# Optimization experiments

Hardware: AMD Instinct MI355X
Metric: run time of the kernel (lower is better)

Reference implementation:

```python
import jax, jax.numpy as jnp
import numpy as np

D, H, DH, W = 1280, 16, 80, 64  # d_model, heads, head_dim, window

def setup_inputs() -> dict:
    key = jax.random.key(0)
    ks = jax.random.split(key, 5)
    s, b = 4096, 8
    x = jax.random.normal(ks[0], (s, b, D), dtype=jnp.float32)
    cu_seqlens = jnp.arange(s // W + 1, dtype=jnp.int64) * W  # ignored by module
    qkv_w = jax.random.normal(ks[1], (3 * D, D), dtype=jnp.float32) * 0.02
    qkv_b = jnp.zeros((3 * D,), dtype=jnp.float32)
    proj_w = jax.random.normal(ks[2], (D, W * DH), dtype=jnp.float32) * 0.02
    proj_b = jnp.zeros((D,), dtype=jnp.float32)
    return {"x": x, "cu_seqlens": cu_seqlens, "qkv_w": qkv_w, "qkv_b": qkv_b,
            "proj_w": proj_w, "proj_b": proj_b}

def reference(x, cu_seqlens, qkv_w, qkv_b, proj_w, proj_b):
    s, b, _ = x.shape
    nw = s // W
    qkv = x @ qkv_w.T + qkv_b                       # (s, b, 3D)
    q, k, v = jnp.split(qkv, 3, axis=2)             # each (s, b, D)
    def prep(t):
        # (s,b,D) -> (b,s,H,DH) -> (b,nw,W,H,DH)
        return t.reshape(s, b, H, DH).transpose(1, 0, 2, 3).reshape(b, nw, W, H, DH)
    q, k, v = prep(q), prep(k), prep(v)
    scale = 1.0 / jnp.sqrt(jnp.array(DH, dtype=x.dtype))
    # Faithful to source: SDPA sees (b, heads=W, seq=H, dim=DH) per window,
    # i.e. attention over the 16-head axis with the 64 window positions as heads.
    scores = jnp.einsum('bnwhd,bnwgd->bnwhg', q, k) * scale   # (b,nw,W,H,H)
    attn = jax.nn.softmax(scores, axis=-1)
    out = jnp.einsum('bnwhg,bnwgd->bnwhd', attn, v)           # (b,nw,W,H,DH)
    # rearrange 'b h s d -> b s h d' per window, then concat over windows (dim=1)
    out = out.transpose(0, 1, 3, 2, 4).reshape(b, nw * H, W * DH)  # (b, nw*H, W*DH)
    out = out.transpose(1, 0, 2)                                    # (nw*H, b, 5120)
    return out @ proj_w.T + proj_b                                  # (nw*H, b, D)
```

## Files before the change

kernel.cpp:

```cpp
#include <hip/hip_runtime.h>
#include <hip/hip_bf16.h>
#include <stdint.h>

typedef __hip_bfloat16 bf16;
typedef __attribute__((ext_vector_type(8))) short short8;
typedef __attribute__((ext_vector_type(4))) float f32x4;

#define S_LEN   4096
#define BATCH   8
#define D_MODEL 1280
#define NHEADS  16
#define DHEAD   80
#define WIN     64
#define NWIN    (S_LEN / WIN)
#define QKV_N   (3 * D_MODEL)
#define ATT_K   (WIN * DHEAD)
#define M_QKV   (S_LEN * BATCH)
#define M_PROJ  (NWIN * NHEADS * BATCH)
#define OUT_ELEMS ((size_t)M_PROJ * D_MODEL)

#define NX4   (M_QKV * D_MODEL / 4)
#define NQW4  (QKV_N * D_MODEL / 4)
#define NPW4  (D_MODEL * ATT_K / 4)
#define NQB4  (QKV_N / 4)
#define NPB4  (D_MODEL / 4)
#define TOT4  (NX4 + NQW4 + NPW4 + NQB4 + NPB4)

__device__ __forceinline__ float bf2f(unsigned short b) {
    union { unsigned int i; float f; } v;
    v.i = ((unsigned int)b) << 16;
    return v.f;
}

__device__ __forceinline__ unsigned short f2bf(float f) {
    __hip_bfloat16 h = __float2bfloat16(f);
    return *reinterpret_cast<unsigned short*>(&h);
}

__global__ void detect_dtype(const unsigned short* __restrict__ x,
                             int* __restrict__ flag) {
    const int lane = threadIdx.x;
    int big = 0;
    for (int j = lane; j < 256; j += 64) {
        unsigned short u = x[2 * j];
        int e = (u >> 7) & 0xFF;
        big += (e >= 135) ? 1 : 0;
    }
#pragma unroll
    for (int m = 1; m < 64; m <<= 1) big += __shfl_xor(big, m, 64);
    if (lane == 0) *flag = (big >= 8) ? 1 : 0;
}

__global__ __launch_bounds__(256) void canon_all(
    const void* __restrict__ x,  const void* __restrict__ qw,
    const void* __restrict__ pw, const void* __restrict__ qb,
    const void* __restrict__ pb,
    bf16* __restrict__ xc, bf16* __restrict__ qwc, bf16* __restrict__ pwc,
    bf16* __restrict__ qbc, bf16* __restrict__ pbc,
    const int* __restrict__ flag) {
    const int f = *flag;
    const long i = (long)blockIdx.x * 256 + threadIdx.x;
    if (i >= TOT4) return;
    const void* src; bf16* dst; long j;
    if (i < NX4)                        { src = x;  dst = xc;  j = i; }
    else if (i < NX4 + NQW4)            { src = qw; dst = qwc; j = i - NX4; }
    else if (i < NX4 + NQW4 + NPW4)     { src = pw; dst = pwc; j = i - NX4 - NQW4; }
    else if (i < NX4 + NQW4 + NPW4 + NQB4) { src = qb; dst = qbc; j = i - NX4 - NQW4 - NPW4; }
    else                                { src = pb; dst = pbc; j = i - NX4 - NQW4 - NPW4 - NQB4; }
    if (f) {
        const float4 v = ((const float4*)src)[j];
        ushort4 o;
        o.x = f2bf(v.x); o.y = f2bf(v.y); o.z = f2bf(v.z); o.w = f2bf(v.w);
        ((ushort4*)dst)[j] = o;
    } else {
        ((ushort4*)dst)[j] = ((const ushort4*)src)[j];
    }
}

__device__ __forceinline__ void gload16(const bf16* g, bf16* l) {
    __builtin_amdgcn_global_load_lds(
        (const __attribute__((address_space(1))) void*)g,
        (__attribute__((address_space(3))) void*)l, 16, 0, 0);
}

__global__ __launch_bounds__(512) void gemm_bt_bias_256(
    const bf16* __restrict__ A, const bf16* __restrict__ B,
    const bf16* __restrict__ bias, void* __restrict__ Cout,
    int M, int N, int K, const int* __restrict__ out_f32)
{
    __shared__ bf16 sA[2][256 * 64];
    __shared__ bf16 sB[2][256 * 64];

    const int t    = threadIdx.x;
    const int lane = t & 63;
    const int wave = t >> 6;
    const int wm   = wave >> 2;
    const int wn   = wave & 3;
    const int quad = lane >> 4;
    const int l16  = lane & 15;
    const int l7   = l16 & 7;

    const int B_nb = N >> 8, B_mb = M >> 8;
    const int mpx  = B_mb >> 3;
    const int gm   = (mpx >= 8) ? 8 : mpx;
    const int gid  = blockIdx.x;
    const int xcd  = gid & 7;
    const int per  = gid >> 3;
    const int grp  = per / (gm * B_nb);
    const int rem  = per - grp * (gm * B_nb);
    const int bn   = rem / gm;
    const int bm   = xcd * mpx + grp * gm + (rem - bn * gm);

    const int trow   = t >> 3;
    const int tchunk = (t & 7) ^ (trow & 7);
    const bf16* Ag = A + (size_t)(bm * 256 + trow) * K + tchunk * 8;
    const bf16* Bg = B + (size_t)(bn * 256 + trow) * K + tchunk * 8;
    const int nt = K >> 6;

#define STAGE(hx, kt_)                                                       \
  do {                                                                       \
    const int _b = (kt_) & 1;                                                \
    if ((hx) == 0 || (hx) == 2) {                                            \
      const int _h = ((hx) == 2) ? 128 : 0;                                  \
      gload16(Ag + (size_t)(_h) * K + (size_t)(kt_) * 64,                    \
              &sA[_b][_h * 64 + wave * 512]);                                \
      gload16(Ag + (size_t)(_h + 64) * K + (size_t)(kt_) * 64,               \
              &sA[_b][(_h + 64) * 64 + wave * 512]);                         \
    } else {                                                                 \
      const int _h = ((hx) == 3) ? 128 : 0;                                  \
      gload16(Bg + (size_t)(_h) * K + (size_t)(kt_) * 64,                    \
              &sB[_b][_h * 64 + wave * 512]);                                \
      gload16(Bg + (size_t)(_h + 64) * K + (size_t)(kt_) * 64,               \
              &sB[_b][(_h + 64) * 64 + wave * 512]);                         \
    }                                                                        \
  } while (0)

    f32x4 acc[8][4];
#pragma unroll
    for (int i = 0; i < 8; ++i)
#pragma unroll
        for (int j = 0; j < 4; ++j)
            acc[i][j] = (f32x4){0.f, 0.f, 0.f, 0.f};

    short8 af[4][2];
    short8 bfr[2][2][2];
    const int pc0 = quad ^ l7;
    const int pc1 = (quad + 4) ^ l7;

#define LDA(mh)                                                              \
  do {                                                                       \
    const bf16* _ab = &sA[cur][((mh) * 128 + wm * 64 + l16) * 64];           \
    _Pragma("unroll")                                                        \
    for (int _i = 0; _i < 4; ++_i) {                                         \
      af[_i][0] = *(const short8*)(_ab + _i * 1024 + pc0 * 8);               \
      af[_i][1] = *(const short8*)(_ab + _i * 1024 + pc1 * 8);               \
    }                                                                        \
  } while (0)

#define LDB(nh)                                                              \
  do {                                                                       \
    const bf16* _bb = &sB[cur][((nh) * 128 + wn * 32 + l16) * 64];           \
    _Pragma("unroll")                                                        \
    for (int _j = 0; _j < 2; ++_j) {                                         \
      bfr[nh][_j][0] = *(const short8*)(_bb + _j * 1024 + pc0 * 8);          \
      bfr[nh][_j][1] = *(const short8*)(_bb + _j * 1024 + pc1 * 8);          \
    }                                                                        \
  } while (0)

#define MFMA_Q(mh, nh)                                                       \
  do {                                                                       \
    _Pragma("unroll")                                                        \
    for (int _i = 0; _i < 4; ++_i)                                           \
      _Pragma("unroll")                                                      \
      for (int _j = 0; _j < 2; ++_j) {                                       \
        acc[(mh) * 4 + _i][(nh) * 2 + _j] =                                  \
            __builtin_amdgcn_mfma_f32_16x16x32_bf16(                         \
                af[_i][0], bfr[nh][_j][0],                                   \
                acc[(mh) * 4 + _i][(nh) * 2 + _j], 0, 0, 0);                 \
        acc[(mh) * 4 + _i][(nh) * 2 + _j] =                                  \
            __builtin_amdgcn_mfma_f32_16x16x32_bf16(                         \
                af[_i][1], bfr[nh][_j][1],                                   \
                acc[(mh) * 4 + _i][(nh) * 2 + _j], 0, 0, 0);                 \
      }                                                                      \
  } while (0)

    STAGE(0, 0); STAGE(1, 0); STAGE(2, 0); STAGE(3, 0);
    if (nt > 1) {
        STAGE(0, 1); STAGE(1, 1); STAGE(2, 1);
        asm volatile("s_waitcnt vmcnt(6)" ::: "memory");
    } else {
        asm volatile("s_waitcnt vmcnt(0)" ::: "memory");
    }
    __builtin_amdgcn_s_barrier();

    int cur = 0;
    for (int kt = 0; kt < nt; ++kt) {
        LDA(0); LDB(0);
        if (kt + 1 < nt) STAGE(3, kt + 1);
        __builtin_amdgcn_s_barrier();
        asm volatile("s_waitcnt lgkmcnt(0)" ::: "memory");
        __builtin_amdgcn_s_setprio(1);
        MFMA_Q(0, 0);
        __builtin_amdgcn_s_setprio(0);
        __builtin_amdgcn_s_barrier();
        LDB(1);
        if (kt + 2 < nt) STAGE(0, kt + 2);
        __builtin_amdgcn_s_barrier();
        asm volatile("s_waitcnt lgkmcnt(0)" ::: "memory");
        __builtin_amdgcn_s_setprio(1);
        MFMA_Q(0, 1);
        __builtin_amdgcn_s_setprio(0);
        __builtin_amdgcn_s_barrier();
        LDA(1);
        if (kt + 2 < nt) STAGE(1, kt + 2);
        __builtin_amdgcn_s_barrier();
        asm volatile("s_waitcnt lgkmcnt(0)" ::: "memory");
        __builtin_amdgcn_s_setprio(1);
        MFMA_Q(1, 1);
        __builtin_amdgcn_s_setprio(0);
        __builtin_amdgcn_s_barrier();
        if (kt + 2 < nt) STAGE(2, kt + 2);
        __builtin_amdgcn_s_barrier();
        __builtin_amdgcn_s_setprio(1);
        MFMA_Q(1, 0);
        __builtin_amdgcn_s_setprio(0);
        if (kt < nt - 2)       asm volatile("s_waitcnt vmcnt(6)" ::: "memory");
        else if (kt == nt - 2) asm volatile("s_waitcnt vmcnt(0)" ::: "memory");
        __builtin_amdgcn_s_barrier();
        cur ^= 1;
    }
#undef STAGE
#undef LDA
#undef LDB
#undef MFMA_Q

    const int outf = out_f32 ? *out_f32 : 0;
    const int crow0 = bm * 256 + wm * 64 + quad * 4;
    const int ccol0 = bn * 256 + wn * 32 + l16;
    if (outf) {
        float* Cf = (float*)Cout;
#pragma unroll
        for (int mh = 0; mh < 2; ++mh)
#pragma unroll
        for (int nh = 0; nh < 2; ++nh)
#pragma unroll
        for (int j = 0; j < 2; ++j) {
            const int col = ccol0 + nh * 128 + j * 16;
            const float bv = bf2f(*(const unsigned short*)&bias[col]);
#pragma unroll
            for (int i = 0; i < 4; ++i) {
                const int row = crow0 + mh * 128 + i * 16;
#pragma unroll
                for (int r = 0; r < 4; ++r)
                    Cf[(size_t)(row + r) * N + col] =
                        acc[mh * 4 + i][nh * 2 + j][r] + bv;
            }
        }
    } else {
        bf16* Cb = (bf16*)Cout;
#pragma unroll
        for (int mh = 0; mh < 2; ++mh)
#pragma unroll
        for (int nh = 0; nh < 2; ++nh)
#pragma unroll
        for (int j = 0; j < 2; ++j) {
            const int col = ccol0 + nh * 128 + j * 16;
            const float bv = bf2f(*(const unsigned short*)&bias[col]);
#pragma unroll
            for (int i = 0; i < 4; ++i) {
                const int row = crow0 + mh * 128 + i * 16;
#pragma unroll
                for (int r = 0; r < 4; ++r)
                    Cb[(size_t)(row + r) * N + col] =
                        __float2bfloat16(acc[mh * 4 + i][nh * 2 + j][r] + bv);
            }
        }
    }
}

__global__ __launch_bounds__(64) void win_attn(
    const bf16* __restrict__ qkv,
    bf16* __restrict__ aout)
{
    __shared__ float sq[16 * 84];
    __shared__ float sk[16 * 84];
    __shared__ float sv[16 * 84];
    __shared__ float swt[16 * 17];

    const int g    = blockIdx.x;
    const int lane = threadIdx.x;
    const int b    = g & 7;
    const int si   = g >> 3;
    const int n    = si >> 6;
    const int w    = si & 63;

    const bf16* row = qkv + (size_t)g * QKV_N;

    for (int c = lane; c < 960; c += 64) {
        const int j = c * 4;
        ushort4 u = *(const ushort4*)(row + j);
        const int seg = j / 1280;
        const int within = j - seg * 1280;
        const int h = within / 80;
        const int d = within - h * 80;
        float* dst = (seg == 0 ? sq : (seg == 1 ? sk : sv)) + h * 84 + d;
        f32x4 v4 = {bf2f(u.x), bf2f(u.y), bf2f(u.z), bf2f(u.w)};
        *(f32x4*)dst = v4;
    }
    __syncthreads();

    const int g16  = lane & 15;
    const int quad = lane >> 4;
    const float scale = 0.11180339887498949f;
#pragma unroll
    for (int p = 0; p < 4; ++p) {
        const int h = quad * 4 + p;
        const f32x4* qv = (const f32x4*)(sq + h * 84);
        const f32x4* kv = (const f32x4*)(sk + g16 * 84);
        float s = 0.f;
#pragma unroll
        for (int d4 = 0; d4 < 20; ++d4) {
            const f32x4 a = qv[d4], bb = kv[d4];
            s += a[0] * bb[0] + a[1] * bb[1] + a[2] * bb[2] + a[3] * bb[3];
        }
        s *= scale;
        float mx = s;
#pragma unroll
        for (int m = 1; m < 16; m <<= 1)
            mx = fmaxf(mx, __shfl_xor(mx, m, 64));
        const float e = __expf(s - mx);
        float sum = e;
#pragma unroll
        for (int m = 1; m < 16; m <<= 1)
            sum += __shfl_xor(sum, m, 64);
        swt[h * 17 + g16] = e / sum;
    }
    __syncthreads();

    const int h2    = lane >> 2;
    const int dbase = (lane & 3) * 20;
    float accv[20];
#pragma unroll
    for (int t = 0; t < 20; ++t) accv[t] = 0.f;
    for (int gg = 0; gg < 16; ++gg) {
        const float wgt = swt[h2 * 17 + gg];
        const float* vp = sv + gg * 84 + dbase;
#pragma unroll
        for (int t = 0; t < 20; ++t) accv[t] += wgt * vp[t];
    }

    const size_t orow = (size_t)((n * 16 + h2) * 8 + b);
    bf16* op = aout + orow * ATT_K + w * 80 + dbase;
#pragma unroll
    for (int t = 0; t < 20; t += 2) {
        const unsigned int packed =
            ((unsigned int)f2bf(accv[t + 1]) << 16) | f2bf(accv[t]);
        *(unsigned int*)(op + t) = packed;
    }
}

extern "C" void kernel_launch(void* const* d_in, const int* in_sizes, int n_in,
                              void* d_out, int out_size, void* d_ws, size_t ws_size,
                              hipStream_t stream) {
    const void* x      = d_in[0];
    const void* qkv_w  = d_in[2];
    const void* qkv_b  = d_in[3];
    const void* proj_w = d_in[4];
    const void* proj_b = d_in[5];

    char* base   = (char*)d_ws;
    int*  flag   = (int*)base;
    bf16* xc     = (bf16*)(base + 256);
    bf16* qkvwc  = xc     + (size_t)M_QKV * D_MODEL;
    bf16* projwc = qkvwc  + (size_t)QKV_N * D_MODEL;
    bf16* qkvbc  = projwc + (size_t)D_MODEL * ATT_K;
    bf16* projbc = qkvbc  + QKV_N;
    bf16* qkv    = projbc + D_MODEL;
    bf16* aout   = xc;

    detect_dtype<<<1, 64, 0, stream>>>((const unsigned short*)x, flag);

    canon_all<<<(TOT4 + 255) / 256, 256, 0, stream>>>(
        x, qkv_w, proj_w, qkv_b, proj_b, xc, qkvwc, projwc, qkvbc, projbc, flag);

    gemm_bt_bias_256<<<(M_QKV / 256) * (QKV_N / 256), 512, 0, stream>>>(
        xc, qkvwc, qkvbc, qkv, M_QKV, QKV_N, D_MODEL, nullptr);

    win_attn<<<M_QKV, 64, 0, stream>>>(qkv, aout);

    gemm_bt_bias_256<<<(M_PROJ / 256) * (D_MODEL / 256), 512, 0, stream>>>(
        aout, projwc, projbc, d_out, M_PROJ, D_MODEL, ATT_K, flag);
}
```

Measured before the change: 962.4 us.

## Simplify GEMM main loop to one barrier per k-tile with full-tile prefetch

Replaces the finely interleaved 8-barrier-per-iteration schedule, which staged quarters of tile kt+2 between MFMA quadrants, with a simpler double-buffered loop. Each iteration waits for all outstanding global loads, does one barrier, reads LDS fragments, issues all four stages of the next tile, then runs all four MFMA quadrants. This cuts barrier and waitcnt overhead. In exchange, prefetch depth drops from about 1.75 tiles to one tile, and a vmcnt(0) wait sits at the top of every iteration, so load latency may be exposed. It also relies on implicit compiler lgkmcnt waits and single-barrier ordering for correctness of LDS buffer reuse.

```diff
diff --git a/kernel.cpp b/kernel.cpp
--- a/kernel.cpp
+++ b/kernel.cpp
@@ -185,48 +185,31 @@
   } while (0)
 
     STAGE(0, 0); STAGE(1, 0); STAGE(2, 0); STAGE(3, 0);
-    if (nt > 1) {
-        STAGE(0, 1); STAGE(1, 1); STAGE(2, 1);
-        asm volatile("s_waitcnt vmcnt(6)" ::: "memory");
-    } else {
-        asm volatile("s_waitcnt vmcnt(0)" ::: "memory");
-    }
-    __builtin_amdgcn_s_barrier();
 
     int cur = 0;
     for (int kt = 0; kt < nt; ++kt) {
-        LDA(0); LDB(0);
-        if (kt + 1 < nt) STAGE(3, kt + 1);
+        asm volatile("s_waitcnt vmcnt(0)" ::: "memory");
         __builtin_amdgcn_s_barrier();
-        asm volatile("s_waitcnt lgkmcnt(0)" ::: "memory");
+        __builtin_amdgcn_sched_barrier(0);
+
+        LDA(0); LDB(0); LDB(1);
+        if (kt + 1 < nt) {
+            STAGE(0, kt + 1); STAGE(1, kt + 1);
+            STAGE(2, kt + 1); STAGE(3, kt + 1);
+        }
+
         __builtin_amdgcn_s_setprio(1);
         MFMA_Q(0, 0);
-        __builtin_amdgcn_s_setprio(0);
-        __builtin_amdgcn_s_barrier();
-        LDB(1);
-        if (kt + 2 < nt) STAGE(0, kt + 2);
-        __builtin_amdgcn_s_barrier();
-        asm volatile("s_waitcnt lgkmcnt(0)" ::: "memory");
-        __builtin_amdgcn_s_setprio(1);
         MFMA_Q(0, 1);
         __builtin_amdgcn_s_setprio(0);
-        __builtin_amdgcn_s_barrier();
+
         LDA(1);
-        if (kt + 2 < nt) STAGE(1, kt + 2);
-        __builtin_amdgcn_s_barrier();
-        asm volatile("s_waitcnt lgkmcnt(0)" ::: "memory");
+
         __builtin_amdgcn_s_setprio(1);
         MFMA_Q(1, 1);
-        __builtin_amdgcn_s_setprio(0);
-        __builtin_amdgcn_s_barrier();
-        if (kt + 2 < nt) STAGE(2, kt + 2);
-        __builtin_amdgcn_s_barrier();
-        __builtin_amdgcn_s_setprio(1);
         MFMA_Q(1, 0);
         __builtin_amdgcn_s_setprio(0);
-        if (kt < nt - 2)       asm volatile("s_waitcnt vmcnt(6)" ::: "memory");
-        else if (kt == nt - 2) asm volatile("s_waitcnt vmcnt(0)" ::: "memory");
-        __builtin_amdgcn_s_barrier();
+
         cur ^= 1;
     }
 #undef STAGE
```

Result: faster. 891.6 us (-7.4%).
